# Kernel optimization log

Measured on AMD Instinct MI355X. Metric: run time of the kernel, lower is better.

Reference implementation:

```python
import jax, jax.numpy as jnp
import numpy as np

N_NODES = 100000


def _mean_agg(x, src, dst, n_nodes):
    # gather neighbor (src) features, segment-sum into destination nodes, divide by in-degree
    summed = jax.ops.segment_sum(x[src], dst, num_segments=n_nodes)  # [N, d]
    deg = jax.ops.segment_sum(jnp.ones_like(dst, dtype=x.dtype), dst, num_segments=n_nodes)
    return summed / jnp.clip(deg, 1.0)[:, None]  # DGL clamps zero in-degree to 1


def _sage_conv(x, src, dst, W_self, W_neigh, b, n_nodes):
    h_neigh = _mean_agg(x, src, dst, n_nodes)
    # DGL SAGEConv(mean): fc_self(h_self) + fc_neigh(h_neigh); single bias
    return x @ W_self + h_neigh @ W_neigh + b


def setup_inputs() -> dict:
    key = jax.random.key(0)
    ks = jax.random.split(key, 8)
    in_f, hid_f, out_f = 64, 64, 16
    n_edges = 1200000
    return {
        "x": jax.random.normal(ks[0], (N_NODES, in_f), dtype=jnp.float32),
        "src": jax.random.randint(ks[1], (n_edges,), 0, N_NODES),
        "dst": jax.random.randint(ks[2], (n_edges,), 0, N_NODES),
        "W1_self": jax.random.normal(ks[3], (in_f, hid_f), dtype=jnp.float32) / np.sqrt(in_f),
        "W1_neigh": jax.random.normal(ks[4], (in_f, hid_f), dtype=jnp.float32) / np.sqrt(in_f),
        "b1": jnp.zeros((hid_f,), dtype=jnp.float32),
        "W2_self": jax.random.normal(ks[5], (hid_f, out_f), dtype=jnp.float32) / np.sqrt(hid_f),
        "W2_neigh": jax.random.normal(ks[6], (hid_f, out_f), dtype=jnp.float32) / np.sqrt(hid_f),
        "b2": jnp.zeros((out_f,), dtype=jnp.float32),
    }


def reference(x, src, dst, W1_self, W1_neigh, b1, W2_self, W2_neigh, b2):
    h = _sage_conv(x, src, dst, W1_self, W1_neigh, b1, N_NODES)
    h = jax.nn.relu(h)
    h = _sage_conv(h, src, dst, W2_self, W2_neigh, b2, N_NODES)
    return h
```

## Files before the change

### kernel.cpp

```cpp
#include <hip/hip_runtime.h>

#define N_NODES 100000
#define N_EDGES 1200000
#define NB 391
#define CHUNK_E 4096
#define NBLK_E 293
#define TOT_H (NB * NBLK_E)
#define NSB2 ((TOT_H + 1023) / 1024)

#define OFF_ROWPTR 0
#define OFF_HISTG  400896
#define OFF_HSCAN  859648
#define OFF_BLK2   1318400
#define OFF_PAIRS  1318912
#define OFF_SORTED 6118912
#define OFF_Y1     10918912
#define OFF_H1     23718912

__device__ __forceinline__ unsigned short f2bf(float f) {
    unsigned u = __float_as_uint(f);
    unsigned r = (u + 0x7fffu + ((u >> 16) & 1u)) >> 16;
    return (unsigned short)r;
}


__global__ __launch_bounds__(256) void chunk_hist_kernel(
    const int* __restrict__ dst, int* __restrict__ hist_g)
{
    __shared__ int h[NB];
    const int e0 = blockIdx.x * CHUNK_E;
    const int e1 = min(e0 + CHUNK_E, N_EDGES);
    for (int i = threadIdx.x; i < NB; i += 256) h[i] = 0;
    __syncthreads();
    for (int e = e0 + threadIdx.x; e < e1; e += 256)
        atomicAdd(&h[dst[e] >> 8], 1);
    __syncthreads();
    for (int i = threadIdx.x; i < NB; i += 256)
        hist_g[i * NBLK_E + blockIdx.x] = h[i];
}

__global__ __launch_bounds__(1024) void scan2_blocks_kernel(
    const int* __restrict__ hist_g, int* __restrict__ hs_scan, int* __restrict__ blk2)
{
    __shared__ int s[1024];
    int i = blockIdx.x * 1024 + threadIdx.x;
    int v = (i < TOT_H) ? hist_g[i] : 0;
    s[threadIdx.x] = v;
    __syncthreads();
    for (int off = 1; off < 1024; off <<= 1) {
        int t = (threadIdx.x >= off) ? s[threadIdx.x - off] : 0;
        __syncthreads();
        s[threadIdx.x] += t;
        __syncthreads();
    }
    if (i < TOT_H) hs_scan[i] = s[threadIdx.x] - v;
    if (threadIdx.x == 1023) blk2[blockIdx.x] = s[1023];
}

__global__ __launch_bounds__(128) void scan2_tops_kernel(int* __restrict__ blk2)
{
    __shared__ int s[128];
    int v = (threadIdx.x < NSB2) ? blk2[threadIdx.x] : 0;
    s[threadIdx.x] = v;
    __syncthreads();
    for (int off = 1; off < 128; off <<= 1) {
        int t = (threadIdx.x >= off) ? s[threadIdx.x - off] : 0;
        __syncthreads();
        s[threadIdx.x] += t;
        __syncthreads();
    }
    if (threadIdx.x < NSB2) blk2[threadIdx.x] = s[threadIdx.x] - v;
}

__global__ __launch_bounds__(256) void pair_scatter_kernel(
    const int* __restrict__ src, const int* __restrict__ dst,
    const int* __restrict__ hs_scan, const int* __restrict__ blk2,
    unsigned* __restrict__ pairs)
{
    __shared__ int base_s[NB];
    __shared__ int cur_s[NB];
    const int b = blockIdx.x;
    const int e0 = b * CHUNK_E;
    const int e1 = min(e0 + CHUNK_E, N_EDGES);

    for (int i = threadIdx.x; i < NB; i += 256) {
        int idx = i * NBLK_E + b;
        base_s[i] = hs_scan[idx] + blk2[idx >> 10];
        cur_s[i] = 0;
    }
    __syncthreads();
    for (int e = e0 + threadIdx.x; e < e1; e += 256) {
        int d = dst[e];
        int bk = d >> 8;
        int pos = base_s[bk] + atomicAdd(&cur_s[bk], 1);
        pairs[pos] = ((unsigned)src[e] << 8) | (unsigned)(d & 255);
    }
}

__global__ __launch_bounds__(256) void bucket_fill_plus_kernel(
    const unsigned* __restrict__ pairs,
    const int* __restrict__ hs_scan, const int* __restrict__ blk2,
    int* __restrict__ row_ptr, int* __restrict__ sorted_src)
{
    __shared__ int hist[256];
    __shared__ int sc[256];
    __shared__ int cur[256];
    const int b = blockIdx.x;
    const int t = threadIdx.x;

    int i0 = b * NBLK_E;
    const int start = hs_scan[i0] + blk2[i0 >> 10];
    int end;
    if (b == NB - 1) end = N_EDGES;
    else {
        int i1 = (b + 1) * NBLK_E;
        end = hs_scan[i1] + blk2[i1 >> 10];
    }

    hist[t] = 0;
    __syncthreads();
    for (int e = start + t; e < end; e += 256)
        atomicAdd(&hist[pairs[e] & 255u], 1);
    __syncthreads();

    int v = hist[t];
    sc[t] = v;
    __syncthreads();
    for (int off = 1; off < 256; off <<= 1) {
        int tv = (t >= off) ? sc[t - off] : 0;
        __syncthreads();
        sc[t] += tv;
        __syncthreads();
    }
    const int excl = sc[t] - v;
    const int node = (b << 8) + t;
    if (node < N_NODES) row_ptr[node] = start + excl;
    if (b == NB - 1 && t == 0) row_ptr[N_NODES] = N_EDGES;
    cur[t] = start + excl;
    __syncthreads();

    for (int e = start + t; e < end; e += 256) {
        unsigned u = pairs[e];
        int pos = atomicAdd(&cur[u & 255u], 1);
        sorted_src[pos] = (int)(u >> 8);
    }
}

__global__ __launch_bounds__(256) void dense1_kernel(
    const float* __restrict__ x,
    const float* __restrict__ Wn, const float* __restrict__ Ws,
    const float* __restrict__ b,
    unsigned short* __restrict__ y1, float* __restrict__ z1)
{
    __shared__ float sx[32 * 64];
    const int t = threadIdx.x;
    const int w = t >> 6;
    const int lane = t & 63;
    const int half = w >> 1;
    const int nsub = (w & 1) * 16;
    const int chunk = blockIdx.x * 32;

    {
        const float4* gx = (const float4*)(x + (size_t)chunk * 64);
        float4* sx4 = (float4*)sx;
        sx4[t] = gx[t];
        sx4[t + 256] = gx[t + 256];
    }

    const float* W = half ? Ws : Wn;
    float wr[64];
#pragma unroll
    for (int k = 0; k < 64; ++k) wr[k] = W[k * 64 + lane];
    const float bj = half ? b[lane] : 0.f;

    __syncthreads();

#pragma unroll 1
    for (int m = 0; m < 16; ++m) {
        const int node = nsub + m;
        const float4* xr = (const float4*)(sx + node * 64);
        float a0 = 0.f, a1 = 0.f, a2 = 0.f, a3 = 0.f;
#pragma unroll
        for (int k4 = 0; k4 < 16; ++k4) {
            float4 v = xr[k4];
            a0 += v.x * wr[4 * k4 + 0];
            a1 += v.y * wr[4 * k4 + 1];
            a2 += v.z * wr[4 * k4 + 2];
            a3 += v.w * wr[4 * k4 + 3];
        }
        const float o = (a0 + a1) + (a2 + a3) + bj;
        const size_t gn = (size_t)(chunk + node);
        if (half) z1[gn * 64 + lane] = o;
        else      y1[gn * 64 + lane] = f2bf(o);
    }
}

__global__ __launch_bounds__(256) void dense2_kernel(
    const float* __restrict__ h1,
    const float* __restrict__ Wn, const float* __restrict__ Ws,
    const float* __restrict__ b,
    float* __restrict__ y2, float* __restrict__ out)
{
    __shared__ float sx[32 * 68];
    const int t = threadIdx.x;
    const int w = t >> 6;
    const int lane = t & 63;
    const int half = w >> 1;
    const int nsub = (w & 1) * 16;
    const int j = lane & 15;
    const int g = lane >> 4;
    const int chunk = blockIdx.x * 32;

    {
        const float4* gx = (const float4*)(h1 + (size_t)chunk * 64);
        float4* sx4 = (float4*)sx;
        int r0 = t >> 4, c0 = t & 15;
        sx4[r0 * 17 + c0] = gx[t];
        sx4[(r0 + 16) * 17 + c0] = gx[t + 256];
    }

    const float* W = half ? Ws : Wn;
    float wr[64];
#pragma unroll
    for (int k = 0; k < 64; ++k) wr[k] = W[k * 16 + j];
    const float bj = half ? b[j] : 0.f;

    __syncthreads();

#pragma unroll 1
    for (int q = 0; q < 4; ++q) {
        const int node = nsub + q * 4 + g;
        const float4* xr = (const float4*)(sx + node * 68);
        float a0 = 0.f, a1 = 0.f, a2 = 0.f, a3 = 0.f;
#pragma unroll
        for (int k4 = 0; k4 < 16; ++k4) {
            float4 v = xr[k4];
            a0 += v.x * wr[4 * k4 + 0];
            a1 += v.y * wr[4 * k4 + 1];
            a2 += v.z * wr[4 * k4 + 2];
            a3 += v.w * wr[4 * k4 + 3];
        }
        const float o = (a0 + a1) + (a2 + a3) + bj;
        const size_t gn = (size_t)(chunk + node);
        if (half) out[gn * 16 + j] = o;
        else      y2[gn * 16 + j] = o;
    }
}


__global__ __launch_bounds__(256) void gather1_kernel(
    const unsigned short* __restrict__ y1,
    const int* __restrict__ row_ptr,
    const int* __restrict__ sorted_src,
    float* __restrict__ h1)
{
    const int w = threadIdx.x >> 6;
    const int lane = threadIdx.x & 63;
    const int n = blockIdx.x * 4 + w;
    const int group = lane >> 4;
    const int fl = lane & 15;

    const int start = row_ptr[n];
    const int deg = row_ptr[n + 1] - start;

    float a0 = 0.f, a1 = 0.f, a2 = 0.f, a3 = 0.f;
    for (int base = 0; base < deg; base += 64) {
        const int m = min(64, deg - base);
        int eid = 0;
        if (lane < m) eid = sorted_src[start + base + lane];
        for (int jj = 0; jj < m; jj += 4) {
            const int idx = jj + group;
            const int s = __shfl(eid, idx);
            if (idx < m) {
                uint2 raw = ((const uint2*)(y1 + (size_t)s * 64))[fl];
                a0 += __uint_as_float(raw.x << 16);
                a1 += __uint_as_float(raw.x & 0xffff0000u);
                a2 += __uint_as_float(raw.y << 16);
                a3 += __uint_as_float(raw.y & 0xffff0000u);
            }
        }
    }
    a0 += __shfl_xor(a0, 16); a1 += __shfl_xor(a1, 16);
    a2 += __shfl_xor(a2, 16); a3 += __shfl_xor(a3, 16);
    a0 += __shfl_xor(a0, 32); a1 += __shfl_xor(a1, 32);
    a2 += __shfl_xor(a2, 32); a3 += __shfl_xor(a3, 32);

    const float invd = 1.0f / (float)max(deg, 1);
    if (group == 0) {
        float4* hp = (float4*)(h1 + (size_t)n * 64);
        float4 z = hp[fl];
        hp[fl] = make_float4(fmaxf(z.x + a0 * invd, 0.f),
                             fmaxf(z.y + a1 * invd, 0.f),
                             fmaxf(z.z + a2 * invd, 0.f),
                             fmaxf(z.w + a3 * invd, 0.f));
    }
}

__global__ __launch_bounds__(256) void gather2_kernel(
    const float* __restrict__ y2,
    const int* __restrict__ row_ptr,
    const int* __restrict__ sorted_src,
    float* __restrict__ out)
{
    const int w = threadIdx.x >> 6;
    const int lane = threadIdx.x & 63;
    const int n = blockIdx.x * 4 + w;
    const int group = lane >> 2;
    const int fl = lane & 3;

    const int start = row_ptr[n];
    const int deg = row_ptr[n + 1] - start;

    float4 acc = make_float4(0.f, 0.f, 0.f, 0.f);
    for (int base = 0; base < deg; base += 64) {
        const int m = min(64, deg - base);
        int eid = 0;
        if (lane < m) eid = sorted_src[start + base + lane];
        for (int jj = 0; jj < m; jj += 16) {
            const int idx = jj + group;
            const int s = __shfl(eid, idx);
            if (idx < m) {
                float4 v = ((const float4*)(y2 + (size_t)s * 16))[fl];
                acc.x += v.x; acc.y += v.y; acc.z += v.z; acc.w += v.w;
            }
        }
    }
#pragma unroll
    for (int d = 4; d <= 32; d <<= 1) {
        acc.x += __shfl_xor(acc.x, d); acc.y += __shfl_xor(acc.y, d);
        acc.z += __shfl_xor(acc.z, d); acc.w += __shfl_xor(acc.w, d);
    }
    const float invd = 1.0f / (float)max(deg, 1);
    if (lane < 4) {
        float4* op = (float4*)(out + (size_t)n * 16);
        float4 z = op[fl];
        op[fl] = make_float4(z.x + acc.x * invd, z.y + acc.y * invd,
                             z.z + acc.z * invd, z.w + acc.w * invd);
    }
}

extern "C" void kernel_launch(void* const* d_in, const int* in_sizes, int n_in,
                              void* d_out, int out_size, void* d_ws, size_t ws_size,
                              hipStream_t stream) {
    const float* x   = (const float*)d_in[0];
    const int*   src = (const int*)d_in[1];
    const int*   dst = (const int*)d_in[2];
    const float* W1s = (const float*)d_in[3];
    const float* W1n = (const float*)d_in[4];
    const float* b1  = (const float*)d_in[5];
    const float* W2s = (const float*)d_in[6];
    const float* W2n = (const float*)d_in[7];
    const float* b2  = (const float*)d_in[8];
    float* out = (float*)d_out;

    char* ws = (char*)d_ws;
    int* row_ptr    = (int*)(ws + OFF_ROWPTR);
    int* hist_g     = (int*)(ws + OFF_HISTG);
    int* hs_scan    = (int*)(ws + OFF_HSCAN);
    int* blk2       = (int*)(ws + OFF_BLK2);
    unsigned* pairs = (unsigned*)(ws + OFF_PAIRS);
    int* sorted_src = (int*)(ws + OFF_SORTED);
    unsigned short* y1 = (unsigned short*)(ws + OFF_Y1);
    float* y2       = (float*)(ws + OFF_Y1);
    float* h1       = (float*)(ws + OFF_H1);

    chunk_hist_kernel<<<NBLK_E, 256, 0, stream>>>(dst, hist_g);
    scan2_blocks_kernel<<<NSB2, 1024, 0, stream>>>(hist_g, hs_scan, blk2);
    scan2_tops_kernel<<<1, 128, 0, stream>>>(blk2);
    pair_scatter_kernel<<<NBLK_E, 256, 0, stream>>>(src, dst, hs_scan, blk2, pairs);
    bucket_fill_plus_kernel<<<NB, 256, 0, stream>>>(pairs, hs_scan, blk2, row_ptr, sorted_src);

    dense1_kernel<<<3125, 256, 0, stream>>>(x, W1n, W1s, b1, y1, h1);
    gather1_kernel<<<N_NODES / 4, 256, 0, stream>>>(y1, row_ptr, sorted_src, h1);

    dense2_kernel<<<3125, 256, 0, stream>>>(h1, W2n, W2s, b2, y2, out);
    gather2_kernel<<<N_NODES / 4, 256, 0, stream>>>(y2, row_ptr, sorted_src, out);
}
```

Baseline: 248.0 us.

## Replace full CSR sort with bucketed pairs and LDS atomic aggregation

Drops the second-level bucket fill that produced a fully sorted CSR, and keeps only the coarse bucket partition of edges with 128 destination nodes per bucket. The aggregation kernels now process each bucket in one block, accumulating neighbor features into shared-memory float atomics and counting degree there, then apply the mean, residual and ReLU. This removes a kernel launch and one pass over the edges, but adds many LDS atomic adds and gives each block only the edges of its bucket to work through.

```diff
diff --git a/kernel.cpp b/kernel.cpp
--- a/kernel.cpp
+++ b/kernel.cpp
@@ -2,20 +2,19 @@
 
 #define N_NODES 100000
 #define N_EDGES 1200000
-#define NB 391
-#define CHUNK_E 4096
-#define NBLK_E 293
+#define BK 128
+#define NB 782
+#define CHUNK_E 8192
+#define NBLK_E 147
 #define TOT_H (NB * NBLK_E)
 #define NSB2 ((TOT_H + 1023) / 1024)
 
-#define OFF_ROWPTR 0
-#define OFF_HISTG  400896
-#define OFF_HSCAN  859648
-#define OFF_BLK2   1318400
-#define OFF_PAIRS  1318912
-#define OFF_SORTED 6118912
-#define OFF_Y1     10918912
-#define OFF_H1     23718912
+#define OFF_HISTG  0
+#define OFF_HSCAN  460032
+#define OFF_BLK2   920064
+#define OFF_PAIRS  920576
+#define OFF_Y1     5720576
+#define OFF_H1     18520576
 
 __device__ __forceinline__ unsigned short f2bf(float f) {
     unsigned u = __float_as_uint(f);
@@ -24,18 +23,18 @@
 }
 
 
-__global__ __launch_bounds__(256) void chunk_hist_kernel(
+__global__ __launch_bounds__(512) void chunk_hist_kernel(
     const int* __restrict__ dst, int* __restrict__ hist_g)
 {
     __shared__ int h[NB];
     const int e0 = blockIdx.x * CHUNK_E;
     const int e1 = min(e0 + CHUNK_E, N_EDGES);
-    for (int i = threadIdx.x; i < NB; i += 256) h[i] = 0;
-    __syncthreads();
-    for (int e = e0 + threadIdx.x; e < e1; e += 256)
-        atomicAdd(&h[dst[e] >> 8], 1);
-    __syncthreads();
-    for (int i = threadIdx.x; i < NB; i += 256)
+    for (int i = threadIdx.x; i < NB; i += 512) h[i] = 0;
+    __syncthreads();
+    for (int e = e0 + threadIdx.x; e < e1; e += 512)
+        atomicAdd(&h[dst[e] >> 7], 1);
+    __syncthreads();
+    for (int i = threadIdx.x; i < NB; i += 512)
         hist_g[i * NBLK_E + blockIdx.x] = h[i];
 }
 
@@ -72,7 +71,7 @@
     if (threadIdx.x < NSB2) blk2[threadIdx.x] = s[threadIdx.x] - v;
 }
 
-__global__ __launch_bounds__(256) void pair_scatter_kernel(
+__global__ __launch_bounds__(512) void pair_scatter_kernel(
     const int* __restrict__ src, const int* __restrict__ dst,
     const int* __restrict__ hs_scan, const int* __restrict__ blk2,
     unsigned* __restrict__ pairs)
@@ -83,68 +82,20 @@
     const int e0 = b * CHUNK_E;
     const int e1 = min(e0 + CHUNK_E, N_EDGES);
 
-    for (int i = threadIdx.x; i < NB; i += 256) {
+    for (int i = threadIdx.x; i < NB; i += 512) {
         int idx = i * NBLK_E + b;
         base_s[i] = hs_scan[idx] + blk2[idx >> 10];
         cur_s[i] = 0;
     }
     __syncthreads();
-    for (int e = e0 + threadIdx.x; e < e1; e += 256) {
+    for (int e = e0 + threadIdx.x; e < e1; e += 512) {
         int d = dst[e];
-        int bk = d >> 8;
+        int bk = d >> 7;
         int pos = base_s[bk] + atomicAdd(&cur_s[bk], 1);
-        pairs[pos] = ((unsigned)src[e] << 8) | (unsigned)(d & 255);
-    }
-}
-
-__global__ __launch_bounds__(256) void bucket_fill_plus_kernel(
-    const unsigned* __restrict__ pairs,
-    const int* __restrict__ hs_scan, const int* __restrict__ blk2,
-    int* __restrict__ row_ptr, int* __restrict__ sorted_src)
-{
-    __shared__ int hist[256];
-    __shared__ int sc[256];
-    __shared__ int cur[256];
-    const int b = blockIdx.x;
-    const int t = threadIdx.x;
-
-    int i0 = b * NBLK_E;
-    const int start = hs_scan[i0] + blk2[i0 >> 10];
-    int end;
-    if (b == NB - 1) end = N_EDGES;
-    else {
-        int i1 = (b + 1) * NBLK_E;
-        end = hs_scan[i1] + blk2[i1 >> 10];
-    }
-
-    hist[t] = 0;
-    __syncthreads();
-    for (int e = start + t; e < end; e += 256)
-        atomicAdd(&hist[pairs[e] & 255u], 1);
-    __syncthreads();
-
-    int v = hist[t];
-    sc[t] = v;
-    __syncthreads();
-    for (int off = 1; off < 256; off <<= 1) {
-        int tv = (t >= off) ? sc[t - off] : 0;
-        __syncthreads();
-        sc[t] += tv;
-        __syncthreads();
-    }
-    const int excl = sc[t] - v;
-    const int node = (b << 8) + t;
-    if (node < N_NODES) row_ptr[node] = start + excl;
-    if (b == NB - 1 && t == 0) row_ptr[N_NODES] = N_EDGES;
-    cur[t] = start + excl;
-    __syncthreads();
-
-    for (int e = start + t; e < end; e += 256) {
-        unsigned u = pairs[e];
-        int pos = atomicAdd(&cur[u & 255u], 1);
-        sorted_src[pos] = (int)(u >> 8);
-    }
-}
+        pairs[pos] = ((unsigned)src[e] << 7) | (unsigned)(d & 127);
+    }
+}
+
 
 __global__ __launch_bounds__(256) void dense1_kernel(
     const float* __restrict__ x,
@@ -248,94 +199,131 @@
 }
 
 
-__global__ __launch_bounds__(256) void gather1_kernel(
+__global__ __launch_bounds__(512) void agg1_kernel(
     const unsigned short* __restrict__ y1,
-    const int* __restrict__ row_ptr,
-    const int* __restrict__ sorted_src,
+    const unsigned* __restrict__ pairs,
+    const int* __restrict__ hs_scan, const int* __restrict__ blk2,
     float* __restrict__ h1)
 {
-    const int w = threadIdx.x >> 6;
-    const int lane = threadIdx.x & 63;
-    const int n = blockIdx.x * 4 + w;
-    const int group = lane >> 4;
-    const int fl = lane & 15;
-
-    const int start = row_ptr[n];
-    const int deg = row_ptr[n + 1] - start;
-
-    float a0 = 0.f, a1 = 0.f, a2 = 0.f, a3 = 0.f;
-    for (int base = 0; base < deg; base += 64) {
-        const int m = min(64, deg - base);
-        int eid = 0;
-        if (lane < m) eid = sorted_src[start + base + lane];
-        for (int jj = 0; jj < m; jj += 4) {
-            const int idx = jj + group;
-            const int s = __shfl(eid, idx);
+    __shared__ float acc[BK * 65];
+    __shared__ int deg[BK];
+    const int b = blockIdx.x;
+    const int t = threadIdx.x;
+    const int lane = t & 63;
+    const int wv = t >> 6;
+    const int g = lane >> 3;
+    const int fl = lane & 7;
+
+    for (int i = t; i < BK * 65; i += 512) acc[i] = 0.f;
+    for (int i = t; i < BK; i += 512) deg[i] = 0;
+
+    const int i0 = b * NBLK_E;
+    const int start = hs_scan[i0] + blk2[i0 >> 10];
+    const int end = (b == NB - 1) ? N_EDGES
+                    : hs_scan[i0 + NBLK_E] + blk2[(i0 + NBLK_E) >> 10];
+    __syncthreads();
+
+    for (int base = start + wv * 64; base < end; base += 512) {
+        const int m = min(64, end - base);
+        unsigned eid = 0;
+        if (lane < m) eid = pairs[base + lane];
+        for (int jj = 0; jj < m; jj += 8) {
+            const int idx = jj + g;
+            const unsigned u = __shfl(eid, idx);
             if (idx < m) {
-                uint2 raw = ((const uint2*)(y1 + (size_t)s * 64))[fl];
-                a0 += __uint_as_float(raw.x << 16);
-                a1 += __uint_as_float(raw.x & 0xffff0000u);
-                a2 += __uint_as_float(raw.y << 16);
-                a3 += __uint_as_float(raw.y & 0xffff0000u);
+                const int s = (int)(u >> 7);
+                const int dl = (int)(u & 127u);
+                uint4 raw = ((const uint4*)(y1 + (size_t)s * 64))[fl];
+                float* a = acc + dl * 65 + fl * 8;
+                atomicAdd(a + 0, __uint_as_float(raw.x << 16));
+                atomicAdd(a + 1, __uint_as_float(raw.x & 0xffff0000u));
+                atomicAdd(a + 2, __uint_as_float(raw.y << 16));
+                atomicAdd(a + 3, __uint_as_float(raw.y & 0xffff0000u));
+                atomicAdd(a + 4, __uint_as_float(raw.z << 16));
+                atomicAdd(a + 5, __uint_as_float(raw.z & 0xffff0000u));
+                atomicAdd(a + 6, __uint_as_float(raw.w << 16));
+                atomicAdd(a + 7, __uint_as_float(raw.w & 0xffff0000u));
+                if (fl == 0) atomicAdd(&deg[dl], 1);
             }
         }
     }
-    a0 += __shfl_xor(a0, 16); a1 += __shfl_xor(a1, 16);
-    a2 += __shfl_xor(a2, 16); a3 += __shfl_xor(a3, 16);
-    a0 += __shfl_xor(a0, 32); a1 += __shfl_xor(a1, 32);
-    a2 += __shfl_xor(a2, 32); a3 += __shfl_xor(a3, 32);
-
-    const float invd = 1.0f / (float)max(deg, 1);
-    if (group == 0) {
-        float4* hp = (float4*)(h1 + (size_t)n * 64);
-        float4 z = hp[fl];
-        hp[fl] = make_float4(fmaxf(z.x + a0 * invd, 0.f),
-                             fmaxf(z.y + a1 * invd, 0.f),
-                             fmaxf(z.z + a2 * invd, 0.f),
-                             fmaxf(z.w + a3 * invd, 0.f));
-    }
-}
-
-__global__ __launch_bounds__(256) void gather2_kernel(
+    __syncthreads();
+
+    const int node0 = b * BK;
+    for (int q = t; q < BK * 16; q += 512) {
+        const int n = q >> 4;
+        const int c = q & 15;
+        const int gn = node0 + n;
+        if (gn >= N_NODES) break;
+        const float invd = 1.0f / (float)max(deg[n], 1);
+        float4* hp = (float4*)(h1 + (size_t)gn * 64);
+        float4 z = hp[c];
+        const float* a = acc + n * 65 + c * 4;
+        hp[c] = make_float4(fmaxf(z.x + a[0] * invd, 0.f),
+                            fmaxf(z.y + a[1] * invd, 0.f),
+                            fmaxf(z.z + a[2] * invd, 0.f),
+                            fmaxf(z.w + a[3] * invd, 0.f));
+    }
+}
+
+__global__ __launch_bounds__(512) void agg2_kernel(
     const float* __restrict__ y2,
-    const int* __restrict__ row_ptr,
-    const int* __restrict__ sorted_src,
+    const unsigned* __restrict__ pairs,
+    const int* __restrict__ hs_scan, const int* __restrict__ blk2,
     float* __restrict__ out)
 {
-    const int w = threadIdx.x >> 6;
-    const int lane = threadIdx.x & 63;
-    const int n = blockIdx.x * 4 + w;
-    const int group = lane >> 2;
+    __shared__ float acc[BK * 17];
+    __shared__ int deg[BK];
+    const int b = blockIdx.x;
+    const int t = threadIdx.x;
+    const int lane = t & 63;
+    const int wv = t >> 6;
+    const int g = lane >> 2;
     const int fl = lane & 3;
 
-    const int start = row_ptr[n];
-    const int deg = row_ptr[n + 1] - start;
-
-    float4 acc = make_float4(0.f, 0.f, 0.f, 0.f);
-    for (int base = 0; base < deg; base += 64) {
-        const int m = min(64, deg - base);
-        int eid = 0;
-        if (lane < m) eid = sorted_src[start + base + lane];
+    for (int i = t; i < BK * 17; i += 512) acc[i] = 0.f;
+    for (int i = t; i < BK; i += 512) deg[i] = 0;
+
+    const int i0 = b * NBLK_E;
+    const int start = hs_scan[i0] + blk2[i0 >> 10];
+    const int end = (b == NB - 1) ? N_EDGES
+                    : hs_scan[i0 + NBLK_E] + blk2[(i0 + NBLK_E) >> 10];
+    __syncthreads();
+
+    for (int base = start + wv * 64; base < end; base += 512) {
+        const int m = min(64, end - base);
+        unsigned eid = 0;
+        if (lane < m) eid = pairs[base + lane];
         for (int jj = 0; jj < m; jj += 16) {
-            const int idx = jj + group;
-            const int s = __shfl(eid, idx);
+            const int idx = jj + g;
+            const unsigned u = __shfl(eid, idx);
             if (idx < m) {
+                const int s = (int)(u >> 7);
+                const int dl = (int)(u & 127u);
                 float4 v = ((const float4*)(y2 + (size_t)s * 16))[fl];
-                acc.x += v.x; acc.y += v.y; acc.z += v.z; acc.w += v.w;
+                float* a = acc + dl * 17 + fl * 4;
+                atomicAdd(a + 0, v.x);
+                atomicAdd(a + 1, v.y);
+                atomicAdd(a + 2, v.z);
+                atomicAdd(a + 3, v.w);
+                if (fl == 0) atomicAdd(&deg[dl], 1);
             }
         }
     }
-#pragma unroll
-    for (int d = 4; d <= 32; d <<= 1) {
-        acc.x += __shfl_xor(acc.x, d); acc.y += __shfl_xor(acc.y, d);
-        acc.z += __shfl_xor(acc.z, d); acc.w += __shfl_xor(acc.w, d);
-    }
-    const float invd = 1.0f / (float)max(deg, 1);
-    if (lane < 4) {
-        float4* op = (float4*)(out + (size_t)n * 16);
-        float4 z = op[fl];
-        op[fl] = make_float4(z.x + acc.x * invd, z.y + acc.y * invd,
-                             z.z + acc.z * invd, z.w + acc.w * invd);
+    __syncthreads();
+
+    const int node0 = b * BK;
+    for (int q = t; q < BK * 4; q += 512) {
+        const int n = q >> 2;
+        const int c = q & 3;
+        const int gn = node0 + n;
+        if (gn >= N_NODES) break;
+        const float invd = 1.0f / (float)max(deg[n], 1);
+        float4* op = (float4*)(out + (size_t)gn * 16);
+        float4 z = op[c];
+        const float* a = acc + n * 17 + c * 4;
+        op[c] = make_float4(z.x + a[0] * invd, z.y + a[1] * invd,
+                            z.z + a[2] * invd, z.w + a[3] * invd);
     }
 }
 
@@ -354,25 +342,22 @@
     float* out = (float*)d_out;
 
     char* ws = (char*)d_ws;
-    int* row_ptr    = (int*)(ws + OFF_ROWPTR);
     int* hist_g     = (int*)(ws + OFF_HISTG);
     int* hs_scan    = (int*)(ws + OFF_HSCAN);
     int* blk2       = (int*)(ws + OFF_BLK2);
     unsigned* pairs = (unsigned*)(ws + OFF_PAIRS);
-    int* sorted_src = (int*)(ws + OFF_SORTED);
     unsigned short* y1 = (unsigned short*)(ws + OFF_Y1);
     float* y2       = (float*)(ws + OFF_Y1);
     float* h1       = (float*)(ws + OFF_H1);
 
-    chunk_hist_kernel<<<NBLK_E, 256, 0, stream>>>(dst, hist_g);
+    chunk_hist_kernel<<<NBLK_E, 512, 0, stream>>>(dst, hist_g);
     scan2_blocks_kernel<<<NSB2, 1024, 0, stream>>>(hist_g, hs_scan, blk2);
     scan2_tops_kernel<<<1, 128, 0, stream>>>(blk2);
-    pair_scatter_kernel<<<NBLK_E, 256, 0, stream>>>(src, dst, hs_scan, blk2, pairs);
-    bucket_fill_plus_kernel<<<NB, 256, 0, stream>>>(pairs, hs_scan, blk2, row_ptr, sorted_src);
+    pair_scatter_kernel<<<NBLK_E, 512, 0, stream>>>(src, dst, hs_scan, blk2, pairs);
 
     dense1_kernel<<<3125, 256, 0, stream>>>(x, W1n, W1s, b1, y1, h1);
-    gather1_kernel<<<N_NODES / 4, 256, 0, stream>>>(y1, row_ptr, sorted_src, h1);
+    agg1_kernel<<<NB, 512, 0, stream>>>(y1, pairs, hs_scan, blk2, h1);
 
     dense2_kernel<<<3125, 256, 0, stream>>>(h1, W2n, W2s, b2, y2, out);
-    gather2_kernel<<<N_NODES / 4, 256, 0, stream>>>(y2, row_ptr, sorted_src, out);
-}
+    agg2_kernel<<<NB, 512, 0, stream>>>(y2, pairs, hs_scan, blk2, out);
+}
```

New measurement: 807.2 us. 3.25x slower.
